# Performance work log

Measured on AMD Instinct MI355X. Metric: run time of the kernel, lower is better.

The kernel has to match this reference:

```python
import jax, jax.numpy as jnp
import numpy as np

N, F_IN, F_OUT, N_HEAD = 4096, 256, 64, 4
EDGE_P = 0.01  # sparsity of the random adjacency


def setup_inputs() -> dict:
    key = jax.random.key(0)
    k_h, k_adj, k_w, k_as, k_ad = jax.random.split(key, 5)
    h = jax.random.normal(k_h, (N, F_IN), dtype=jnp.float32)
    # random boolean adjacency with self-loops so every softmax row is valid
    adj = jax.random.uniform(k_adj, (N, N)) < EDGE_P
    adj = adj | jnp.eye(N, dtype=bool)
    # xavier_uniform-style params
    lim_w = float(np.sqrt(6.0 / (F_IN + F_OUT)))
    lim_a = float(np.sqrt(6.0 / (F_OUT + 1)))
    w = jax.random.uniform(k_w, (N_HEAD, F_IN, F_OUT), minval=-lim_w, maxval=lim_w, dtype=jnp.float32)
    a_src = jax.random.uniform(k_as, (N_HEAD, F_OUT, 1), minval=-lim_a, maxval=lim_a, dtype=jnp.float32)
    a_dst = jax.random.uniform(k_ad, (N_HEAD, F_OUT, 1), minval=-lim_a, maxval=lim_a, dtype=jnp.float32)
    bias = jnp.zeros((F_OUT,), dtype=jnp.float32)
    return {"h": h, "adj": adj, "w": w, "a_src": a_src, "a_dst": a_dst, "bias": bias}


def reference(h, adj, w, a_src, a_dst, bias):
    # h_prime[k] = h @ w[k]  -> [H, n, f_out]
    h_prime = jnp.einsum('nf,hfo->hno', h, w)
    # attention logits: attn[k,i,j] = src[k,i] + dst[k,j]
    src = jnp.einsum('hno,ho->hn', h_prime, a_src[..., 0])  # [H, n]
    dst = jnp.einsum('hno,ho->hn', h_prime, a_dst[..., 0])  # [H, n]
    scores = src[:, :, None] + dst[:, None, :]              # [H, n, n]
    scores = jnp.where(scores >= 0, scores, 0.2 * scores)   # leaky_relu(0.2)
    neg = jnp.asarray(jnp.finfo(scores.dtype).min, scores.dtype)
    scores = jnp.where(adj[None, :, :], scores, neg)
    attn = jax.nn.softmax(scores, axis=-1)                  # [H, n, n]
    out = jnp.einsum('hij,hjo->iho', attn, h_prime)         # [n, H, f_out]
    return out + bias
```

## Files before the change

### kernel.cpp

```cpp
#include <hip/hip_runtime.h>

#define NN 4096
#define FIN 256
#define FOUT 64
#define NH 4
#define CAP 128

typedef __attribute__((ext_vector_type(8))) short bf16x8;
typedef __attribute__((ext_vector_type(4))) float f32x4;

__device__ __forceinline__ unsigned short f2bf(float f) {
    unsigned u = __float_as_uint(f);
    u = (u + 0x7fff + ((u >> 16) & 1)) >> 16;
    return (unsigned short)u;
}
__device__ __forceinline__ float bf2f(unsigned short s) {
    return __uint_as_float((unsigned)s << 16);
}
__device__ __forceinline__ int mbcnt64(unsigned long long m) {
    return __builtin_amdgcn_mbcnt_hi((unsigned)(m >> 32),
           __builtin_amdgcn_mbcnt_lo((unsigned)m, 0));
}

__global__ __launch_bounds__(256) void gat_mfma(
    const float* __restrict__ h, const float* __restrict__ w,
    const float* __restrict__ a_src, const float* __restrict__ a_dst,
    unsigned short* __restrict__ hb, float* __restrict__ sd)
{
    const int b = blockIdx.x, t = threadIdx.x;
    const int wv = t >> 6, lane = t & 63;
    const int head = b & 3, n0 = (b >> 2) * 64;
    const int lrow = lane & 15, lk8 = lane >> 4;

    __shared__ bf16x8 bfrag[2048];

    const float* hrow = h + (size_t)(n0 + wv * 16 + lrow) * FIN + lk8 * 8;
    bf16x8 a[8];
#pragma unroll
    for (int ks = 0; ks < 8; ++ks) {
        const float4 v0 = *(const float4*)(hrow + ks * 32);
        const float4 v1 = *(const float4*)(hrow + ks * 32 + 4);
        union { bf16x8 v; unsigned short s[8]; } u;
        u.s[0] = f2bf(v0.x); u.s[1] = f2bf(v0.y);
        u.s[2] = f2bf(v0.z); u.s[3] = f2bf(v0.w);
        u.s[4] = f2bf(v1.x); u.s[5] = f2bf(v1.y);
        u.s[6] = f2bf(v1.z); u.s[7] = f2bf(v1.w);
        a[ks] = u.v;
    }

#pragma unroll
    for (int i = 0; i < 8; ++i) {
        const int g = t + i * 256;
        const int lg = g & 63, ks = (g >> 6) & 7, nt = g >> 9;
        const int col = nt * 16 + (lg & 15);
        const int kbase = ks * 32 + (lg >> 4) * 8;
        const float* wp = w + ((size_t)head * FIN + kbase) * FOUT + col;
        union { bf16x8 v; unsigned short s[8]; } u;
#pragma unroll
        for (int j = 0; j < 8; ++j) u.s[j] = f2bf(wp[j * FOUT]);
        bfrag[g] = u.v;
    }
    __syncthreads();

    f32x4 acc[4] = {{0.f,0.f,0.f,0.f},{0.f,0.f,0.f,0.f},
                    {0.f,0.f,0.f,0.f},{0.f,0.f,0.f,0.f}};
#pragma unroll
    for (int ks = 0; ks < 8; ++ks) {
#pragma unroll
        for (int nt = 0; nt < 4; ++nt)
            acc[nt] = __builtin_amdgcn_mfma_f32_16x16x32_bf16(
                          a[ks], bfrag[(nt * 8 + ks) * 64 + lane], acc[nt], 0, 0, 0);
    }

    const int mbase = n0 + wv * 16 + lk8 * 4;
#pragma unroll
    for (int nt = 0; nt < 4; ++nt)
#pragma unroll
        for (int r = 0; r < 4; ++r)
            hb[((size_t)head * NN + mbase + r) * FOUT + nt * 16 + lrow] =
                f2bf(acc[nt][r]);

    float as_nt[4], ad_nt[4];
#pragma unroll
    for (int nt = 0; nt < 4; ++nt) {
        as_nt[nt] = a_src[head * FOUT + nt * 16 + lrow];
        ad_nt[nt] = a_dst[head * FOUT + nt * 16 + lrow];
    }
    float psr[4] = {0.f,0.f,0.f,0.f}, pdr[4] = {0.f,0.f,0.f,0.f};
#pragma unroll
    for (int nt = 0; nt < 4; ++nt)
#pragma unroll
        for (int r = 0; r < 4; ++r) {
            psr[r] = fmaf(acc[nt][r], as_nt[nt], psr[r]);
            pdr[r] = fmaf(acc[nt][r], ad_nt[nt], pdr[r]);
        }
#pragma unroll
    for (int r = 0; r < 4; ++r)
#pragma unroll
        for (int off = 1; off <= 8; off <<= 1) {
            psr[r] += __shfl_xor(psr[r], off, 64);
            pdr[r] += __shfl_xor(pdr[r], off, 64);
        }
    if (lrow == 0)
#pragma unroll
        for (int r = 0; r < 4; ++r) {
            sd[(size_t)(mbase + r) * 8 + head]     = psr[r];
            sd[(size_t)(mbase + r) * 8 + 4 + head] = pdr[r];
        }
}

__global__ __launch_bounds__(256) void gat_attn(
    const int* __restrict__ adj, const unsigned short* __restrict__ hb,
    const float* __restrict__ sd, const float* __restrict__ bias,
    float* __restrict__ out)
{
    const int i = blockIdx.x, t = threadIdx.x, wv = t >> 6, lane = t & 63;

    __shared__ int   idx_l[CAP];
    __shared__ float sc[NH][CAP];
    __shared__ int   ccnt[16];
    __shared__ float inv_sum[NH];

    const int4* arow = (const int4*)(adj + (size_t)i * NN);
    int4 a[4];
#pragma unroll
    for (int it = 0; it < 4; ++it) a[it] = arow[wv * 256 + it * 64 + lane];

    int myoff[4];
#pragma unroll
    for (int it = 0; it < 4; ++it) {
        const unsigned long long b0 = __ballot(a[it].x != 0);
        const unsigned long long b1 = __ballot(a[it].y != 0);
        const unsigned long long b2 = __ballot(a[it].z != 0);
        const unsigned long long b3 = __ballot(a[it].w != 0);
        myoff[it] = mbcnt64(b0) + mbcnt64(b1) + mbcnt64(b2) + mbcnt64(b3);
        if (lane == 0)
            ccnt[wv * 4 + it] = __popcll(b0) + __popcll(b1) +
                                __popcll(b2) + __popcll(b3);
    }
    __syncthreads();

    int cb[4];
    int s = 0;
#pragma unroll
    for (int k = 0; k < 16; ++k) {
        if ((k >> 2) == wv) cb[k & 3] = s;
        s += ccnt[k];
    }
    const int count = min(s, CAP);
    const int cpad  = (count + 7) & ~7;

#pragma unroll
    for (int it = 0; it < 4; ++it) {
        int p = cb[it] + myoff[it];
        const int col0 = (wv * 256 + it * 64 + lane) * 4;
        if (a[it].x) { if (p < CAP) idx_l[p] = col0;     ++p; }
        if (a[it].y) { if (p < CAP) idx_l[p] = col0 + 1; ++p; }
        if (a[it].z) { if (p < CAP) idx_l[p] = col0 + 2; ++p; }
        if (a[it].w) { if (p < CAP) idx_l[p] = col0 + 3; ++p; }
    }
    __syncthreads();

    if (t < count) {
        const int j = idx_l[t];
        const float4 sv = *(const float4*)(sd + (size_t)i * 8);
        const float4 dv = *(const float4*)(sd + (size_t)j * 8 + 4);
        const float s0 = sv.x + dv.x, s1 = sv.y + dv.y;
        const float s2 = sv.z + dv.z, s3 = sv.w + dv.w;
        sc[0][t] = (s0 >= 0.f) ? s0 : 0.2f * s0;
        sc[1][t] = (s1 >= 0.f) ? s1 : 0.2f * s1;
        sc[2][t] = (s2 >= 0.f) ? s2 : 0.2f * s2;
        sc[3][t] = (s3 >= 0.f) ? s3 : 0.2f * s3;
    } else if (t < cpad) {
        idx_l[t] = 0;
#pragma unroll
        for (int hh = 0; hh < NH; ++hh) sc[hh][t] = 0.f;
    }
    __syncthreads();

    {
        float m = -3.4e38f;
        for (int p = lane; p < count; p += 64) m = fmaxf(m, sc[wv][p]);
#pragma unroll
        for (int off = 32; off >= 1; off >>= 1) m = fmaxf(m, __shfl_xor(m, off, 64));
        float e = 0.f;
        for (int p = lane; p < count; p += 64) {
            const float v = __expf(sc[wv][p] - m);
            sc[wv][p] = v;
            e += v;
        }
#pragma unroll
        for (int off = 32; off >= 1; off >>= 1) e += __shfl_xor(e, off, 64);
        if (lane == 0) inv_sum[wv] = 1.f / e;
    }
    __syncthreads();

    float accv = 0.f;
    const unsigned short* hp = hb + (size_t)(wv * NN) * FOUT + lane;
    for (int p0 = 0; p0 < cpad; p0 += 8) {
        int jj[8]; unsigned short vv[8]; float ww[8];
#pragma unroll
        for (int k = 0; k < 8; ++k) jj[k] = idx_l[p0 + k];
#pragma unroll
        for (int k = 0; k < 8; ++k) vv[k] = hp[(size_t)jj[k] * FOUT];
#pragma unroll
        for (int k = 0; k < 8; ++k) ww[k] = sc[wv][p0 + k];
#pragma unroll
        for (int k = 0; k < 8; ++k) accv = fmaf(ww[k], bf2f(vv[k]), accv);
    }
    out[(size_t)i * (NH * FOUT) + wv * FOUT + lane] = accv * inv_sum[wv] + bias[lane];
}

extern "C" void kernel_launch(void* const* d_in, const int* in_sizes, int n_in,
                              void* d_out, int out_size, void* d_ws, size_t ws_size,
                              hipStream_t stream) {
    const float* h     = (const float*)d_in[0];
    const int*   adj   = (const int*)d_in[1];
    const float* w     = (const float*)d_in[2];
    const float* a_src = (const float*)d_in[3];
    const float* a_dst = (const float*)d_in[4];
    const float* bias  = (const float*)d_in[5];
    float* out = (float*)d_out;

    unsigned short* hb = (unsigned short*)d_ws;
    float* sd          = (float*)(hb + (size_t)NH * NN * FOUT);

    gat_mfma<<<256, 256, 0, stream>>>(h, w, a_src, a_dst, hb, sd);
    gat_attn<<<NN, 256, 0, stream>>>(adj, hb, sd, bias, out);
}
```

Baseline: 35.27 us.

## Split h-prime projection across more blocks and stage W transposed in LDS

The projection kernel now uses 512 blocks of 32 nodes instead of 256 blocks of 64. Within a block, wave pairs split the 64 output columns. W is loaded with coalesced float4 reads and stored transposed in LDS with a padded row stride, so each MFMA B fragment becomes one vector LDS read. The partial attention dot products from the two waves of a pair are combined through LDS before writing to sd. This adds parallelism and fixes the strided W loads, but duplicates W staging across twice as many blocks, and the padded 258-element rows may give misaligned 16-byte LDS reads.

```diff
diff --git a/kernel.cpp b/kernel.cpp
--- a/kernel.cpp
+++ b/kernel.cpp
@@ -5,6 +5,7 @@
 #define FOUT 64
 #define NH 4
 #define CAP 128
+#define WROW 258
 
 typedef __attribute__((ext_vector_type(8))) short bf16x8;
 typedef __attribute__((ext_vector_type(4))) float f32x4;
@@ -22,19 +23,31 @@
            __builtin_amdgcn_mbcnt_lo((unsigned)m, 0));
 }
 
-__global__ __launch_bounds__(256) void gat_mfma(
+__global__ __launch_bounds__(256) void gat_hprime(
     const float* __restrict__ h, const float* __restrict__ w,
     const float* __restrict__ a_src, const float* __restrict__ a_dst,
     unsigned short* __restrict__ hb, float* __restrict__ sd)
 {
     const int b = blockIdx.x, t = threadIdx.x;
+    const int head = b & 3, n0 = (b >> 2) * 32;
     const int wv = t >> 6, lane = t & 63;
-    const int head = b & 3, n0 = (b >> 2) * 64;
     const int lrow = lane & 15, lk8 = lane >> 4;
 
-    __shared__ bf16x8 bfrag[2048];
-
-    const float* hrow = h + (size_t)(n0 + wv * 16 + lrow) * FIN + lk8 * 8;
+    __shared__ __align__(16) unsigned short ws[64 * WROW];
+    __shared__ float sdbuf[2][2][16][2];
+
+#pragma unroll
+    for (int i = 0; i < 16; ++i) {
+        const int k  = (t >> 4) + i * 16;
+        const int o4 = (t & 15) * 4;
+        const float4 v = *(const float4*)(w + ((size_t)head * FIN + k) * FOUT + o4);
+        ws[(o4 + 0) * WROW + k] = f2bf(v.x);
+        ws[(o4 + 1) * WROW + k] = f2bf(v.y);
+        ws[(o4 + 2) * WROW + k] = f2bf(v.z);
+        ws[(o4 + 3) * WROW + k] = f2bf(v.w);
+    }
+
+    const float* hrow = h + (size_t)(n0 + (wv >> 1) * 16 + lrow) * FIN + lk8 * 8;
     bf16x8 a[8];
 #pragma unroll
     for (int ks = 0; ks < 8; ++ks) {
@@ -47,48 +60,37 @@
         u.s[6] = f2bf(v1.z); u.s[7] = f2bf(v1.w);
         a[ks] = u.v;
     }
-
-#pragma unroll
-    for (int i = 0; i < 8; ++i) {
-        const int g = t + i * 256;
-        const int lg = g & 63, ks = (g >> 6) & 7, nt = g >> 9;
-        const int col = nt * 16 + (lg & 15);
-        const int kbase = ks * 32 + (lg >> 4) * 8;
-        const float* wp = w + ((size_t)head * FIN + kbase) * FOUT + col;
-        union { bf16x8 v; unsigned short s[8]; } u;
-#pragma unroll
-        for (int j = 0; j < 8; ++j) u.s[j] = f2bf(wp[j * FOUT]);
-        bfrag[g] = u.v;
-    }
-    __syncthreads();
-
-    f32x4 acc[4] = {{0.f,0.f,0.f,0.f},{0.f,0.f,0.f,0.f},
-                    {0.f,0.f,0.f,0.f},{0.f,0.f,0.f,0.f}};
+    __syncthreads();
+
+    const int obase = (wv & 1) * 32;
+    f32x4 acc[2] = {{0.f,0.f,0.f,0.f},{0.f,0.f,0.f,0.f}};
 #pragma unroll
     for (int ks = 0; ks < 8; ++ks) {
 #pragma unroll
-        for (int nt = 0; nt < 4; ++nt)
-            acc[nt] = __builtin_amdgcn_mfma_f32_16x16x32_bf16(
-                          a[ks], bfrag[(nt * 8 + ks) * 64 + lane], acc[nt], 0, 0, 0);
-    }
-
-    const int mbase = n0 + wv * 16 + lk8 * 4;
-#pragma unroll
-    for (int nt = 0; nt < 4; ++nt)
+        for (int nt = 0; nt < 2; ++nt) {
+            const bf16x8 bf = *(const bf16x8*)
+                &ws[(obase + nt * 16 + lrow) * WROW + ks * 32 + lk8 * 8];
+            acc[nt] = __builtin_amdgcn_mfma_f32_16x16x32_bf16(a[ks], bf, acc[nt], 0, 0, 0);
+        }
+    }
+
+    const int mbase = n0 + (wv >> 1) * 16 + lk8 * 4;
+#pragma unroll
+    for (int nt = 0; nt < 2; ++nt)
 #pragma unroll
         for (int r = 0; r < 4; ++r)
-            hb[((size_t)head * NN + mbase + r) * FOUT + nt * 16 + lrow] =
+            hb[((size_t)head * NN + mbase + r) * FOUT + obase + nt * 16 + lrow] =
                 f2bf(acc[nt][r]);
 
-    float as_nt[4], ad_nt[4];
-#pragma unroll
-    for (int nt = 0; nt < 4; ++nt) {
-        as_nt[nt] = a_src[head * FOUT + nt * 16 + lrow];
-        ad_nt[nt] = a_dst[head * FOUT + nt * 16 + lrow];
+    float as_nt[2], ad_nt[2];
+#pragma unroll
+    for (int nt = 0; nt < 2; ++nt) {
+        as_nt[nt] = a_src[head * FOUT + obase + nt * 16 + lrow];
+        ad_nt[nt] = a_dst[head * FOUT + obase + nt * 16 + lrow];
     }
     float psr[4] = {0.f,0.f,0.f,0.f}, pdr[4] = {0.f,0.f,0.f,0.f};
 #pragma unroll
-    for (int nt = 0; nt < 4; ++nt)
+    for (int nt = 0; nt < 2; ++nt)
 #pragma unroll
         for (int r = 0; r < 4; ++r) {
             psr[r] = fmaf(acc[nt][r], as_nt[nt], psr[r]);
@@ -104,9 +106,20 @@
     if (lrow == 0)
 #pragma unroll
         for (int r = 0; r < 4; ++r) {
-            sd[(size_t)(mbase + r) * 8 + head]     = psr[r];
-            sd[(size_t)(mbase + r) * 8 + 4 + head] = pdr[r];
-        }
+            sdbuf[wv >> 1][wv & 1][lk8 * 4 + r][0] = psr[r];
+            sdbuf[wv >> 1][wv & 1][lk8 * 4 + r][1] = pdr[r];
+        }
+    __syncthreads();
+    if ((wv & 1) == 0 && lrow == 0) {
+        const int p = wv >> 1;
+#pragma unroll
+        for (int r = 0; r < 4; ++r) {
+            const int n = lk8 * 4 + r;
+            const int node = n0 + p * 16 + n;
+            sd[(size_t)node * 8 + head]     = sdbuf[p][0][n][0] + sdbuf[p][1][n][0];
+            sd[(size_t)node * 8 + 4 + head] = sdbuf[p][0][n][1] + sdbuf[p][1][n][1];
+        }
+    }
 }
 
 __global__ __launch_bounds__(256) void gat_attn(
@@ -225,6 +238,6 @@
     unsigned short* hb = (unsigned short*)d_ws;
     float* sd          = (float*)(hb + (size_t)NH * NN * FOUT);
 
-    gat_mfma<<<256, 256, 0, stream>>>(h, w, a_src, a_dst, hb, sd);
+    gat_hprime<<<512, 256, 0, stream>>>(h, w, a_src, a_dst, hb, sd);
     gat_attn<<<NN, 256, 0, stream>>>(adj, hb, sd, bias, out);
 }
```

Measured after the change: 36.15 us. 2.5% more time.
